# Optimization experiments

Hardware: AMD Instinct MI355X
Metric: run time of the kernel (lower is better)

Reference implementation:

```python
import jax, jax.numpy as jnp
import numpy as np

EMBED = 768
B, S = 8, 2048

def setup_inputs() -> dict:
    key = jax.random.key(0)
    k1, k2, k3, k4 = jax.random.split(key, 4)
    x = jax.random.normal(k1, (B, S, EMBED), dtype=jnp.float32)
    scale = 1.0 / np.sqrt(EMBED)
    Wv = jax.random.normal(k2, (EMBED, EMBED), dtype=jnp.float32) * scale
    Wk = jax.random.normal(k3, (EMBED, EMBED), dtype=jnp.float32) * scale
    Wq = jax.random.normal(k4, (EMBED, EMBED), dtype=jnp.float32) * scale
    mask = jnp.ones((B, S, S), dtype=jnp.int32)
    return {"x": x, "Wv": Wv, "Wk": Wk, "Wq": Wq, "mask": mask}

def reference(x, Wv, Wk, Wq, mask):
    # nn.Linear(E, E, bias=False): y = x @ W.T
    values = jnp.einsum('bse,fe->bsf', x, Wv)
    keys = jnp.einsum('bse,fe->bsf', x, Wk)
    queries = jnp.einsum('bse,fe->bsf', x, Wq)
    energy = jnp.einsum('bqd,bkd->bqk', queries, keys)  # [B,S,S]
    energy = jnp.where(mask == 0, jnp.float32(-1e20), energy)
    attention = jax.nn.softmax(energy / jnp.sqrt(jnp.float32(EMBED)), axis=2)
    out = jnp.einsum('bqk,bkd->bqd', attention, values)
    return out
```

## Files before the change

kernel.cpp:

```cpp
#include <hip/hip_runtime.h>
#include <stdint.h>

#define EMB 768
#define NBATCH 8
#define SEQ 2048
#define M_TOT (NBATCH*SEQ)

using bf16x8 = __attribute__((ext_vector_type(8))) short;
using f32x4  = __attribute__((ext_vector_type(4))) float;

__device__ __forceinline__ short f2bf(float f) {
  __bf16 h = (__bf16)f;
  return __builtin_bit_cast(short, h);
}
__device__ __forceinline__ short f2h(float f) {
  _Float16 h = (_Float16)f;
  return __builtin_bit_cast(short, h);
}
__device__ __forceinline__ float h2f(short s) {
  return (float)__builtin_bit_cast(_Float16, s);
}
__device__ __forceinline__ f32x4 MFMA(bf16x8 a, bf16x8 b, f32x4 c) {
  return __builtin_amdgcn_mfma_f32_16x16x32_bf16(a, b, c, 0, 0, 0);
}
#define GLOAD_LDS16(g, l) __builtin_amdgcn_global_load_lds( \
    (const __attribute__((address_space(1))) unsigned int*)(g), \
    (__attribute__((address_space(3))) unsigned int*)(l), 16, 0, 0)

__global__ __launch_bounds__(256) void cvt_all(
    const float* __restrict__ x, const float* __restrict__ Wq,
    const float* __restrict__ Wk, const float* __restrict__ Wv,
    short* __restrict__ xb, short* __restrict__ Wb)
{
  const size_t NXU = (size_t)M_TOT * EMB / 8;
  const size_t NWU = (size_t)EMB * EMB / 8;
  const size_t total = NXU + 3 * NWU;
  for (size_t u = (size_t)blockIdx.x * 256 + threadIdx.x; u < total;
       u += (size_t)gridDim.x * 256) {
    const float* src; short* dst; size_t off;
    if (u < NXU)            { src = x;  dst = xb;                          off = u; }
    else if (u < NXU+NWU)   { src = Wq; dst = Wb;                          off = u - NXU; }
    else if (u < NXU+2*NWU) { src = Wk; dst = Wb + (size_t)EMB*EMB;        off = u - NXU - NWU; }
    else                    { src = Wv; dst = Wb + (size_t)2*EMB*EMB;      off = u - NXU - 2*NWU; }
    float4 a = reinterpret_cast<const float4*>(src)[off*2];
    float4 c = reinterpret_cast<const float4*>(src)[off*2+1];
    bf16x8 o;
    o[0]=f2bf(a.x); o[1]=f2bf(a.y); o[2]=f2bf(a.z); o[3]=f2bf(a.w);
    o[4]=f2bf(c.x); o[5]=f2bf(c.y); o[6]=f2bf(c.z); o[7]=f2bf(c.w);
    reinterpret_cast<bf16x8*>(dst)[off] = o;
  }
}

#define GEMM_STAGE(As, Bs, asrc, bsrc, lda, ldb)                             \
  {                                                                          \
    _Pragma("unroll")                                                        \
    for (int i = 0; i < 4; ++i) {                                            \
      int slot = i*256 + t;                                                  \
      int row = slot >> 3, g = slot & 7;                                     \
      int gs = (g ^ (row & 7)) << 3;                                         \
      GLOAD_LDS16((asrc) + (size_t)row*(lda) + gs,                           \
                  (char*)&As[0] + (size_t)(i*256 + w*64)*16);                \
      GLOAD_LDS16((bsrc) + (size_t)row*(ldb) + gs,                           \
                  (char*)&Bs[0] + (size_t)(i*256 + w*64)*16);                \
    }                                                                        \
  }

#define GEMM_MFMA(As, Bs)                                                    \
  {                                                                          \
    _Pragma("unroll")                                                        \
    for (int ks = 0; ks < 2; ++ks) {                                         \
      bf16x8 a[4], bb[4];                                                    \
      _Pragma("unroll")                                                      \
      for (int i = 0; i < 4; ++i) {                                          \
        int ra = wm*64 + i*16 + l15;                                         \
        a[i]  = *reinterpret_cast<const bf16x8*>(                            \
                  &As[ra*64 + (((ks*4 + l4) ^ (ra & 7)) << 3)]);             \
        int rb = wn*64 + i*16 + l15;                                         \
        bb[i] = *reinterpret_cast<const bf16x8*>(                            \
                  &Bs[rb*64 + (((ks*4 + l4) ^ (rb & 7)) << 3)]);             \
      }                                                                      \
      _Pragma("unroll")                                                      \
      for (int mi = 0; mi < 4; ++mi)                                         \
        _Pragma("unroll")                                                    \
        for (int ni = 0; ni < 4; ++ni)                                       \
          acc[mi][ni] = MFMA(a[mi], bb[ni], acc[mi][ni]);                    \
    }                                                                        \
  }

__global__ __launch_bounds__(256, 4) void qkv_gemm(
    const short* __restrict__ xb, const short* __restrict__ Wb,
    short* __restrict__ Qb, short* __restrict__ Kb, short* __restrict__ Vt)
{
  __shared__ short As[128*64];
  __shared__ short Bs[128*64];

  const int bid = blockIdx.x;
  const int nb = (bid & 7) * 288 + (bid >> 3);
  const int g = nb / 12, r = nb % 12;
  const int bm = (g / 6) * 4 + r / 3;
  const int bn = (g % 6) * 3 + r % 3;
  const int mbase = bm * 128;

  const short* asrc = xb + (size_t)mbase * EMB;
  const short* bsrc = Wb + (size_t)bn * 128 * EMB;

  const int t = threadIdx.x, lane = t & 63, w = t >> 6;
  const int wm = w >> 1, wn = w & 1, l15 = lane & 15, l4 = lane >> 4;

  f32x4 acc[4][4] = {};

  GEMM_STAGE(As, Bs, asrc, bsrc, EMB, EMB);
  for (int kk = 0; kk < 12; ++kk) {
    asm volatile("s_waitcnt vmcnt(0)" ::: "memory");
    __syncthreads();
    GEMM_MFMA(As, Bs);
    if (kk < 11) {
      __syncthreads();
      GEMM_STAGE(As, Bs, asrc + (kk+1)*64, bsrc + (kk+1)*64, EMB, EMB);
    }
  }

#pragma unroll
  for (int mi = 0; mi < 4; ++mi) {
#pragma unroll
    for (int ni = 0; ni < 4; ++ni) {
      int f = bn * 128 + wn * 64 + ni * 16 + l15;
      int m0 = mbase + wm * 64 + mi * 16 + l4 * 4;
      f32x4 v = acc[mi][ni];
      if (f < 1536) {
        short* dst = (f < 768) ? (Qb + f) : (Kb + (f - 768));
#pragma unroll
        for (int j = 0; j < 4; ++j)
          dst[(size_t)(m0 + j) * EMB] = f2bf(v[j]);
      } else {
        int f2 = f - 1536, bb2 = m0 >> 11, s = m0 & 2047;
        short4 pk = make_short4(f2bf(v[0]), f2bf(v[1]), f2bf(v[2]), f2bf(v[3]));
        *reinterpret_cast<short4*>(&Vt[((size_t)bb2 * EMB + f2) * SEQ + s]) = pk;
      }
    }
  }
}

__global__ __launch_bounds__(256, 4) void energy(
    const short* __restrict__ Qb, const short* __restrict__ Kb,
    short* __restrict__ S)
{
  __shared__ short As[128*64];
  __shared__ short Bs[128*64];

  const int bid = blockIdx.x;
  const int nb = (bid & 7) * 256 + (bid >> 3);
  const int b = nb >> 8;
  const int idx = nb & 255;
  const int sup = idx >> 4, sub = idx & 15;
  const int qt = (sup >> 2) * 4 + (sub >> 2);
  const int kt = (sup & 3) * 4 + (sub & 3);

  const short* asrc = Qb + ((size_t)b*SEQ + qt*128) * EMB;
  const short* bsrc = Kb + ((size_t)b*SEQ + kt*128) * EMB;

  const int t = threadIdx.x, lane = t & 63, w = t >> 6;
  const int wm = w >> 1, wn = w & 1, l15 = lane & 15, l4 = lane >> 4;

  f32x4 acc[4][4] = {};

  GEMM_STAGE(As, Bs, asrc, bsrc, EMB, EMB);
  for (int kk = 0; kk < 12; ++kk) {
    asm volatile("s_waitcnt vmcnt(0)" ::: "memory");
    __syncthreads();
    GEMM_MFMA(As, Bs);
    if (kk < 11) {
      __syncthreads();
      GEMM_STAGE(As, Bs, asrc + (kk+1)*64, bsrc + (kk+1)*64, EMB, EMB);
    }
  }

  const float SCL = 1.4426950408889634f / 27.712812921102035f;
  short* srow = S + (size_t)b * SEQ * SEQ;
#pragma unroll
  for (int mi = 0; mi < 4; ++mi) {
#pragma unroll
    for (int j = 0; j < 4; ++j) {
      int q = qt*128 + wm*64 + mi*16 + l4*4 + j;
#pragma unroll
      for (int ni = 0; ni < 4; ++ni) {
        int k = kt*128 + wn*64 + ni*16 + l15;
        srow[(size_t)q*SEQ + k] = f2h(acc[mi][ni][j] * SCL);
      }
    }
  }
}

__global__ __launch_bounds__(256, 8) void softmax_rows(
    short* __restrict__ S, const int* __restrict__ mask,
    float* __restrict__ invl)
{
  const int w = threadIdx.x >> 6, lane = threadIdx.x & 63;
  const int r = blockIdx.x * 4 + w;
  short* row = S + (size_t)r * SEQ;
  const int4* mrow = reinterpret_cast<const int4*>(mask + (size_t)r * SEQ);

  float f[32];
#pragma unroll
  for (int c = 0; c < 4; ++c) {
    bf16x8 v = *reinterpret_cast<const bf16x8*>(&row[c*512 + lane*8]);
    int4 m0 = mrow[(c*512 + lane*8) >> 2];
    int4 m1 = mrow[((c*512 + lane*8) >> 2) + 1];
    f[c*8+0] = m0.x ? h2f(v[0]) : -30000.0f;
    f[c*8+1] = m0.y ? h2f(v[1]) : -30000.0f;
    f[c*8+2] = m0.z ? h2f(v[2]) : -30000.0f;
    f[c*8+3] = m0.w ? h2f(v[3]) : -30000.0f;
    f[c*8+4] = m1.x ? h2f(v[4]) : -30000.0f;
    f[c*8+5] = m1.y ? h2f(v[5]) : -30000.0f;
    f[c*8+6] = m1.z ? h2f(v[6]) : -30000.0f;
    f[c*8+7] = m1.w ? h2f(v[7]) : -30000.0f;
  }
  float m = -3.0e38f;
#pragma unroll
  for (int i = 0; i < 32; ++i) m = fmaxf(m, f[i]);
#pragma unroll
  for (int off = 32; off >= 1; off >>= 1) m = fmaxf(m, __shfl_xor(m, off));
  float sum = 0.f;
#pragma unroll
  for (int i = 0; i < 32; ++i) {
    f[i] = __builtin_amdgcn_exp2f(f[i] - m);
    sum += f[i];
  }
#pragma unroll
  for (int off = 32; off >= 1; off >>= 1) sum += __shfl_xor(sum, off);

#pragma unroll
  for (int c = 0; c < 4; ++c) {
    bf16x8 o;
#pragma unroll
    for (int j = 0; j < 8; ++j) o[j] = f2bf(f[c*8 + j]);
    *reinterpret_cast<bf16x8*>(&row[c*512 + lane*8]) = o;
  }
  if (lane == 0) invl[r] = 1.0f / sum;
}

__global__ __launch_bounds__(256, 4) void pv(
    const short* __restrict__ P, const short* __restrict__ Vt,
    const float* __restrict__ invl, float* __restrict__ out)
{
  __shared__ short As[128*64];
  __shared__ short Bs[128*64];

  const int bid = blockIdx.x;
  const int nb = (bid & 7) * 96 + (bid >> 3);
  const int b = nb / 96;
  const int idx = nb % 96;
  const int qt = idx / 6, dt = idx % 6;

  const short* asrc = P  + ((size_t)b*SEQ + qt*128) * SEQ;
  const short* bsrc = Vt + ((size_t)b*EMB + dt*128) * SEQ;

  const int t = threadIdx.x, lane = t & 63, w = t >> 6;
  const int wm = w >> 1, wn = w & 1, l15 = lane & 15, l4 = lane >> 4;

  f32x4 acc[4][4] = {};

  GEMM_STAGE(As, Bs, asrc, bsrc, SEQ, SEQ);
  for (int kk = 0; kk < 32; ++kk) {
    asm volatile("s_waitcnt vmcnt(0)" ::: "memory");
    __syncthreads();
    GEMM_MFMA(As, Bs);
    if (kk < 31) {
      __syncthreads();
      GEMM_STAGE(As, Bs, asrc + (kk+1)*64, bsrc + (kk+1)*64, SEQ, SEQ);
    }
  }

#pragma unroll
  for (int mi = 0; mi < 4; ++mi) {
#pragma unroll
    for (int j = 0; j < 4; ++j) {
      int q = qt*128 + wm*64 + mi*16 + l4*4 + j;
      float il = invl[b*SEQ + q];
      float* orow = out + ((size_t)b*SEQ + q) * EMB;
#pragma unroll
      for (int ni = 0; ni < 4; ++ni) {
        int d = dt*128 + wn*64 + ni*16 + l15;
        orow[d] = acc[mi][ni][j] * il;
      }
    }
  }
}

extern "C" void kernel_launch(void* const* d_in, const int* in_sizes, int n_in,
                              void* d_out, int out_size, void* d_ws, size_t ws_size,
                              hipStream_t stream)
{
  (void)in_sizes; (void)n_in; (void)out_size; (void)ws_size;
  const float* x  = (const float*)d_in[0];
  const float* Wv = (const float*)d_in[1];
  const float* Wk = (const float*)d_in[2];
  const float* Wq = (const float*)d_in[3];
  const int* mask = (const int*)d_in[4];
  float* out = (float*)d_out;

  short* Qb = (short*)d_ws;
  short* Kb = Qb + (size_t)M_TOT * EMB;
  short* Vt = Kb + (size_t)M_TOT * EMB;
  short* S  = Vt + (size_t)M_TOT * EMB;
  float* invl = (float*)(S + (size_t)NBATCH * SEQ * SEQ);
  short* xb = S;
  short* Wb = S + (size_t)M_TOT * EMB;

  cvt_all<<<dim3(2048), dim3(256), 0, stream>>>(x, Wq, Wk, Wv, xb, Wb);
  qkv_gemm<<<dim3(2304), dim3(256), 0, stream>>>(xb, Wb, Qb, Kb, Vt);
  energy<<<dim3(2048), dim3(256), 0, stream>>>(Qb, Kb, S);
  softmax_rows<<<dim3(4096), dim3(256), 0, stream>>>(S, mask, invl);
  pv<<<dim3(768), dim3(256), 0, stream>>>(S, Vt, invl, out);
}
```

Before: 245.8 us.

## Use 256x256 double-buffered GEMM tiles with phased loads and MFMA priority

The QKV projection, energy and PV GEMMs now use 512-thread blocks computing 256x256 output tiles, replacing 128x128 tiles. Operands are double-buffered in 128KB of dynamic LDS, and each K step is split into four quarter phases. Each phase issues the next tile's half-loads while MFMAs run, with s_setprio raised around the MFMAs. The aim is more operand reuse per byte loaded and overlap of global-to-LDS traffic with compute. In exchange, only one block fits per CU, grids are much smaller (PV has only 192 blocks), and the kernels depend on a large dynamic LDS launch succeeding.

```diff
diff --git a/kernel.cpp b/kernel.cpp
--- a/kernel.cpp
+++ b/kernel.cpp
@@ -38,10 +38,10 @@
   for (size_t u = (size_t)blockIdx.x * 256 + threadIdx.x; u < total;
        u += (size_t)gridDim.x * 256) {
     const float* src; short* dst; size_t off;
-    if (u < NXU)            { src = x;  dst = xb;                          off = u; }
-    else if (u < NXU+NWU)   { src = Wq; dst = Wb;                          off = u - NXU; }
-    else if (u < NXU+2*NWU) { src = Wk; dst = Wb + (size_t)EMB*EMB;        off = u - NXU - NWU; }
-    else                    { src = Wv; dst = Wb + (size_t)2*EMB*EMB;      off = u - NXU - 2*NWU; }
+    if (u < NXU)            { src = x;  dst = xb;                     off = u; }
+    else if (u < NXU+NWU)   { src = Wq; dst = Wb;                     off = u - NXU; }
+    else if (u < NXU+2*NWU) { src = Wk; dst = Wb + (size_t)EMB*EMB;   off = u - NXU - NWU; }
+    else                    { src = Wv; dst = Wb + (size_t)2*EMB*EMB; off = u - NXU - 2*NWU; }
     float4 a = reinterpret_cast<const float4*>(src)[off*2];
     float4 c = reinterpret_cast<const float4*>(src)[off*2+1];
     bf16x8 o;
@@ -51,143 +51,152 @@
   }
 }
 
-#define GEMM_STAGE(As, Bs, asrc, bsrc, lda, ldb)                             \
-  {                                                                          \
-    _Pragma("unroll")                                                        \
-    for (int i = 0; i < 4; ++i) {                                            \
-      int slot = i*256 + t;                                                  \
-      int row = slot >> 3, g = slot & 7;                                     \
-      int gs = (g ^ (row & 7)) << 3;                                         \
-      GLOAD_LDS16((asrc) + (size_t)row*(lda) + gs,                           \
-                  (char*)&As[0] + (size_t)(i*256 + w*64)*16);                \
-      GLOAD_LDS16((bsrc) + (size_t)row*(ldb) + gs,                           \
-                  (char*)&Bs[0] + (size_t)(i*256 + w*64)*16);                \
-    }                                                                        \
-  }
-
-#define GEMM_MFMA(As, Bs)                                                    \
-  {                                                                          \
-    _Pragma("unroll")                                                        \
-    for (int ks = 0; ks < 2; ++ks) {                                         \
-      bf16x8 a[4], bb[4];                                                    \
-      _Pragma("unroll")                                                      \
-      for (int i = 0; i < 4; ++i) {                                          \
-        int ra = wm*64 + i*16 + l15;                                         \
-        a[i]  = *reinterpret_cast<const bf16x8*>(                            \
-                  &As[ra*64 + (((ks*4 + l4) ^ (ra & 7)) << 3)]);             \
-        int rb = wn*64 + i*16 + l15;                                         \
-        bb[i] = *reinterpret_cast<const bf16x8*>(                            \
-                  &Bs[rb*64 + (((ks*4 + l4) ^ (rb & 7)) << 3)]);             \
-      }                                                                      \
-      _Pragma("unroll")                                                      \
-      for (int mi = 0; mi < 4; ++mi)                                         \
-        _Pragma("unroll")                                                    \
-        for (int ni = 0; ni < 4; ++ni)                                       \
-          acc[mi][ni] = MFMA(a[mi], bb[ni], acc[mi][ni]);                    \
-    }                                                                        \
-  }
-
-__global__ __launch_bounds__(256, 4) void qkv_gemm(
+#define STAGE_HALF(ldsb, src, ld, k0, h)                                      \
+  { _Pragma("unroll") for (int i_ = 0; i_ < 2; ++i_) {                        \
+      int slot_ = i_*512 + t;                                                 \
+      int row_ = (h)*128 + (slot_ >> 3), g_ = slot_ & 7;                      \
+      GLOAD_LDS16((src) + (size_t)row_*(ld) + (k0) + ((g_ ^ (row_ & 7)) << 3),\
+                  (ldsb) + (h)*16384 + (size_t)(i_*512 + w*64)*16); } }
+
+#define PHASE(mh, nh, W, ...)                                                 \
+  {                                                                           \
+    bf16x8 af_[2][4], bfr_[2][2];                                             \
+    _Pragma("unroll") for (int ks_ = 0; ks_ < 2; ++ks_) {                     \
+      _Pragma("unroll") for (int mi_ = 0; mi_ < 4; ++mi_) {                   \
+        int r_ = (mh)*128 + wm*64 + mi_*16 + l15;                             \
+        af_[ks_][mi_] = *reinterpret_cast<const bf16x8*>(                     \
+            Ar + r_*64 + (((ks_*4 + l4) ^ (r_ & 7)) << 3));                   \
+      }                                                                       \
+      _Pragma("unroll") for (int ni_ = 0; ni_ < 2; ++ni_) {                   \
+        int r_ = (nh)*128 + wn*32 + ni_*16 + l15;                             \
+        bfr_[ks_][ni_] = *reinterpret_cast<const bf16x8*>(                    \
+            Br + r_*64 + (((ks_*4 + l4) ^ (r_ & 7)) << 3));                   \
+      }                                                                       \
+    }                                                                         \
+    __VA_ARGS__                                                               \
+    asm volatile("s_waitcnt vmcnt(" #W ")" ::: "memory");                     \
+    asm volatile("s_barrier" ::: "memory");                                   \
+    __builtin_amdgcn_s_setprio(1);                                            \
+    _Pragma("unroll") for (int ks_ = 0; ks_ < 2; ++ks_)                       \
+      _Pragma("unroll") for (int mi_ = 0; mi_ < 4; ++mi_)                     \
+        _Pragma("unroll") for (int ni_ = 0; ni_ < 2; ++ni_)                   \
+          acc[mh][nh][mi_][ni_] =                                             \
+              MFMA(af_[ks_][mi_], bfr_[ks_][ni_], acc[mh][nh][mi_][ni_]);     \
+    __builtin_amdgcn_s_setprio(0);                                            \
+    asm volatile("s_barrier" ::: "memory");                                   \
+  }
+
+#define GEMM_PRO_BODY(asrc, bsrc, lda, ldb, NT)                               \
+  short* const A0p = (short*)smem;                                            \
+  short* const B0p = (short*)(smem + 32768);                                  \
+  short* const A1p = (short*)(smem + 65536);                                  \
+  short* const B1p = (short*)(smem + 98304);                                  \
+  f32x4 acc[2][2][4][2] = {};                                                 \
+  STAGE_HALF((char*)A0p, asrc, lda, 0, 0);                                    \
+  STAGE_HALF((char*)B0p, bsrc, ldb, 0, 0);                                    \
+  STAGE_HALF((char*)B0p, bsrc, ldb, 0, 1);                                    \
+  STAGE_HALF((char*)A0p, asrc, lda, 0, 1);                                    \
+  asm volatile("s_waitcnt vmcnt(4)" ::: "memory");                            \
+  asm volatile("s_barrier" ::: "memory");                                     \
+  for (int T = 0; T < (NT) - 1; ++T) {                                        \
+    short* Ar = (T & 1) ? A1p : A0p;                                          \
+    short* Br = (T & 1) ? B1p : B0p;                                          \
+    char* Aw = (char*)((T & 1) ? A0p : A1p);                                  \
+    char* Bw = (char*)((T & 1) ? B0p : B1p);                                  \
+    const int nk = (T + 1) * 64;                                              \
+    PHASE(0,0, 4, STAGE_HALF(Aw, asrc, lda, nk, 0))                           \
+    PHASE(0,1, 4, STAGE_HALF(Bw, bsrc, ldb, nk, 0))                           \
+    PHASE(1,0, 4, STAGE_HALF(Bw, bsrc, ldb, nk, 1))                           \
+    PHASE(1,1, 4, STAGE_HALF(Aw, asrc, lda, nk, 1))                           \
+  }                                                                           \
+  {                                                                           \
+    short* Ar = (((NT)-1) & 1) ? A1p : A0p;                                   \
+    short* Br = (((NT)-1) & 1) ? B1p : B0p;                                   \
+    asm volatile("s_waitcnt vmcnt(0)" ::: "memory");     \
+    asm volatile("s_barrier" ::: "memory");                                   \
+    PHASE(0,0, 0)                                                             \
+    PHASE(0,1, 0)                                                             \
+    PHASE(1,0, 0)                                                             \
+    PHASE(1,1, 0)                                                             \
+  }
+
+__global__ __launch_bounds__(512, 2) void qkv_gemm(
     const short* __restrict__ xb, const short* __restrict__ Wb,
     short* __restrict__ Qb, short* __restrict__ Kb, short* __restrict__ Vt)
 {
-  __shared__ short As[128*64];
-  __shared__ short Bs[128*64];
+  extern __shared__ char smem[];
+  const int t = threadIdx.x, lane = t & 63, w = t >> 6;
+  const int wm = w >> 2, wn = w & 3, l15 = lane & 15, l4 = lane >> 4;
 
   const int bid = blockIdx.x;
-  const int nb = (bid & 7) * 288 + (bid >> 3);
-  const int g = nb / 12, r = nb % 12;
-  const int bm = (g / 6) * 4 + r / 3;
-  const int bn = (g % 6) * 3 + r % 3;
-  const int mbase = bm * 128;
-
-  const short* asrc = xb + (size_t)mbase * EMB;
-  const short* bsrc = Wb + (size_t)bn * 128 * EMB;
-
-  const int t = threadIdx.x, lane = t & 63, w = t >> 6;
-  const int wm = w >> 1, wn = w & 1, l15 = lane & 15, l4 = lane >> 4;
-
-  f32x4 acc[4][4] = {};
-
-  GEMM_STAGE(As, Bs, asrc, bsrc, EMB, EMB);
-  for (int kk = 0; kk < 12; ++kk) {
-    asm volatile("s_waitcnt vmcnt(0)" ::: "memory");
-    __syncthreads();
-    GEMM_MFMA(As, Bs);
-    if (kk < 11) {
-      __syncthreads();
-      GEMM_STAGE(As, Bs, asrc + (kk+1)*64, bsrc + (kk+1)*64, EMB, EMB);
+  const int nb = (bid & 7) * 72 + (bid >> 3);
+  const int bm = nb / 9, bn = nb % 9;
+
+  const short* asrc = xb + (size_t)bm * 256 * EMB;
+  const short* bsrc = Wb + (size_t)bn * 256 * EMB;
+
+  GEMM_PRO_BODY(asrc, bsrc, EMB, EMB, 12)
+
+#pragma unroll
+  for (int mh = 0; mh < 2; ++mh)
+#pragma unroll
+  for (int nh = 0; nh < 2; ++nh)
+#pragma unroll
+  for (int mi = 0; mi < 4; ++mi)
+#pragma unroll
+  for (int ni = 0; ni < 2; ++ni) {
+    int f  = bn*256 + nh*128 + wn*32 + ni*16 + l15;
+    int m0 = bm*256 + mh*128 + wm*64 + mi*16 + l4*4;
+    f32x4 v = acc[mh][nh][mi][ni];
+    if (f < 1536) {
+      short* dst = (f < 768) ? (Qb + f) : (Kb + (f - 768));
+#pragma unroll
+      for (int j = 0; j < 4; ++j)
+        dst[(size_t)(m0 + j) * EMB] = f2bf(v[j]);
+    } else {
+      int f2 = f - 1536, bb2 = m0 >> 11, s = m0 & 2047;
+      short4 pk = make_short4(f2bf(v[0]), f2bf(v[1]), f2bf(v[2]), f2bf(v[3]));
+      *reinterpret_cast<short4*>(&Vt[((size_t)bb2 * EMB + f2) * SEQ + s]) = pk;
     }
   }
-
-#pragma unroll
-  for (int mi = 0; mi < 4; ++mi) {
-#pragma unroll
-    for (int ni = 0; ni < 4; ++ni) {
-      int f = bn * 128 + wn * 64 + ni * 16 + l15;
-      int m0 = mbase + wm * 64 + mi * 16 + l4 * 4;
-      f32x4 v = acc[mi][ni];
-      if (f < 1536) {
-        short* dst = (f < 768) ? (Qb + f) : (Kb + (f - 768));
-#pragma unroll
-        for (int j = 0; j < 4; ++j)
-          dst[(size_t)(m0 + j) * EMB] = f2bf(v[j]);
-      } else {
-        int f2 = f - 1536, bb2 = m0 >> 11, s = m0 & 2047;
-        short4 pk = make_short4(f2bf(v[0]), f2bf(v[1]), f2bf(v[2]), f2bf(v[3]));
-        *reinterpret_cast<short4*>(&Vt[((size_t)bb2 * EMB + f2) * SEQ + s]) = pk;
-      }
-    }
-  }
-}
-
-__global__ __launch_bounds__(256, 4) void energy(
+}
+
+__global__ __launch_bounds__(512, 2) void energy(
     const short* __restrict__ Qb, const short* __restrict__ Kb,
     short* __restrict__ S)
 {
-  __shared__ short As[128*64];
-  __shared__ short Bs[128*64];
+  extern __shared__ char smem[];
+  const int t = threadIdx.x, lane = t & 63, w = t >> 6;
+  const int wm = w >> 2, wn = w & 3, l15 = lane & 15, l4 = lane >> 4;
 
   const int bid = blockIdx.x;
-  const int nb = (bid & 7) * 256 + (bid >> 3);
-  const int b = nb >> 8;
-  const int idx = nb & 255;
-  const int sup = idx >> 4, sub = idx & 15;
-  const int qt = (sup >> 2) * 4 + (sub >> 2);
-  const int kt = (sup & 3) * 4 + (sub & 3);
-
-  const short* asrc = Qb + ((size_t)b*SEQ + qt*128) * EMB;
-  const short* bsrc = Kb + ((size_t)b*SEQ + kt*128) * EMB;
-
-  const int t = threadIdx.x, lane = t & 63, w = t >> 6;
-  const int wm = w >> 1, wn = w & 1, l15 = lane & 15, l4 = lane >> 4;
-
-  f32x4 acc[4][4] = {};
-
-  GEMM_STAGE(As, Bs, asrc, bsrc, EMB, EMB);
-  for (int kk = 0; kk < 12; ++kk) {
-    asm volatile("s_waitcnt vmcnt(0)" ::: "memory");
-    __syncthreads();
-    GEMM_MFMA(As, Bs);
-    if (kk < 11) {
-      __syncthreads();
-      GEMM_STAGE(As, Bs, asrc + (kk+1)*64, bsrc + (kk+1)*64, EMB, EMB);
-    }
-  }
+  const int nb = (bid & 7) * 64 + (bid >> 3);
+  const int b = nb >> 6;
+  const int idx = nb & 63;
+  const int sup = idx >> 2, sub = idx & 3;
+  const int qt = (sup >> 2) * 2 + (sub >> 1);
+  const int kt = (sup & 3) * 2 + (sub & 1);
+
+  const short* asrc = Qb + ((size_t)b*SEQ + qt*256) * EMB;
+  const short* bsrc = Kb + ((size_t)b*SEQ + kt*256) * EMB;
+
+  GEMM_PRO_BODY(asrc, bsrc, EMB, EMB, 12)
 
   const float SCL = 1.4426950408889634f / 27.712812921102035f;
   short* srow = S + (size_t)b * SEQ * SEQ;
 #pragma unroll
-  for (int mi = 0; mi < 4; ++mi) {
-#pragma unroll
-    for (int j = 0; j < 4; ++j) {
-      int q = qt*128 + wm*64 + mi*16 + l4*4 + j;
-#pragma unroll
-      for (int ni = 0; ni < 4; ++ni) {
-        int k = kt*128 + wn*64 + ni*16 + l15;
-        srow[(size_t)q*SEQ + k] = f2h(acc[mi][ni][j] * SCL);
-      }
-    }
+  for (int mh = 0; mh < 2; ++mh)
+#pragma unroll
+  for (int nh = 0; nh < 2; ++nh)
+#pragma unroll
+  for (int mi = 0; mi < 4; ++mi)
+#pragma unroll
+  for (int ni = 0; ni < 2; ++ni)
+#pragma unroll
+  for (int j = 0; j < 4; ++j) {
+    int q = qt*256 + mh*128 + wm*64 + mi*16 + l4*4 + j;
+    int k = kt*256 + nh*128 + wn*32 + ni*16 + l15;
+    srow[(size_t)q*SEQ + k] = f2h(acc[mh][nh][mi][ni][j] * SCL);
   }
 }
 
@@ -239,50 +248,40 @@
   if (lane == 0) invl[r] = 1.0f / sum;
 }
 
-__global__ __launch_bounds__(256, 4) void pv(
+__global__ __launch_bounds__(512, 2) void pv(
     const short* __restrict__ P, const short* __restrict__ Vt,
     const float* __restrict__ invl, float* __restrict__ out)
 {
-  __shared__ short As[128*64];
-  __shared__ short Bs[128*64];
+  extern __shared__ char smem[];
+  const int t = threadIdx.x, lane = t & 63, w = t >> 6;
+  const int wm = w >> 2, wn = w & 3, l15 = lane & 15, l4 = lane >> 4;
 
   const int bid = blockIdx.x;
-  const int nb = (bid & 7) * 96 + (bid >> 3);
-  const int b = nb / 96;
-  const int idx = nb % 96;
-  const int qt = idx / 6, dt = idx % 6;
-
-  const short* asrc = P  + ((size_t)b*SEQ + qt*128) * SEQ;
-  const short* bsrc = Vt + ((size_t)b*EMB + dt*128) * SEQ;
-
-  const int t = threadIdx.x, lane = t & 63, w = t >> 6;
-  const int wm = w >> 1, wn = w & 1, l15 = lane & 15, l4 = lane >> 4;
-
-  f32x4 acc[4][4] = {};
-
-  GEMM_STAGE(As, Bs, asrc, bsrc, SEQ, SEQ);
-  for (int kk = 0; kk < 32; ++kk) {
-    asm volatile("s_waitcnt vmcnt(0)" ::: "memory");
-    __syncthreads();
-    GEMM_MFMA(As, Bs);
-    if (kk < 31) {
-      __syncthreads();
-      GEMM_STAGE(As, Bs, asrc + (kk+1)*64, bsrc + (kk+1)*64, SEQ, SEQ);
-    }
-  }
-
-#pragma unroll
-  for (int mi = 0; mi < 4; ++mi) {
-#pragma unroll
-    for (int j = 0; j < 4; ++j) {
-      int q = qt*128 + wm*64 + mi*16 + l4*4 + j;
-      float il = invl[b*SEQ + q];
-      float* orow = out + ((size_t)b*SEQ + q) * EMB;
-#pragma unroll
-      for (int ni = 0; ni < 4; ++ni) {
-        int d = dt*128 + wn*64 + ni*16 + l15;
-        orow[d] = acc[mi][ni][j] * il;
-      }
+  const int nb = (bid & 7) * 24 + (bid >> 3);
+  const int b = nb / 24;
+  const int idx = nb % 24;
+  const int qt = idx / 3, dt = idx % 3;
+
+  const short* asrc = P  + ((size_t)b*SEQ + qt*256) * SEQ;
+  const short* bsrc = Vt + ((size_t)b*EMB + dt*256) * SEQ;
+
+  GEMM_PRO_BODY(asrc, bsrc, SEQ, SEQ, 32)
+
+#pragma unroll
+  for (int mh = 0; mh < 2; ++mh)
+#pragma unroll
+  for (int nh = 0; nh < 2; ++nh)
+#pragma unroll
+  for (int mi = 0; mi < 4; ++mi)
+#pragma unroll
+  for (int j = 0; j < 4; ++j) {
+    int q = qt*256 + mh*128 + wm*64 + mi*16 + l4*4 + j;
+    float il = invl[b*SEQ + q];
+    float* orow = out + ((size_t)b*SEQ + q) * EMB;
+#pragma unroll
+    for (int ni = 0; ni < 2; ++ni) {
+      int d = dt*256 + nh*128 + wn*32 + ni*16 + l15;
+      orow[d] = acc[mh][nh][mi][ni][j] * il;
     }
   }
 }
@@ -308,8 +307,8 @@
   short* Wb = S + (size_t)M_TOT * EMB;
 
   cvt_all<<<dim3(2048), dim3(256), 0, stream>>>(x, Wq, Wk, Wv, xb, Wb);
-  qkv_gemm<<<dim3(2304), dim3(256), 0, stream>>>(xb, Wb, Qb, Kb, Vt);
-  energy<<<dim3(2048), dim3(256), 0, stream>>>(Qb, Kb, S);
+  qkv_gemm<<<dim3(576), dim3(512), 131072, stream>>>(xb, Wb, Qb, Kb, Vt);
+  energy<<<dim3(512), dim3(512), 131072, stream>>>(Qb, Kb, S);
   softmax_rows<<<dim3(4096), dim3(256), 0, stream>>>(S, mask, invl);
-  pv<<<dim3(768), dim3(256), 0, stream>>>(S, Vt, invl, out);
-}
+  pv<<<dim3(192), dim3(512), 131072, stream>>>(S, Vt, invl, out);
+}
```

New measurement: 272.1 us. 1.11x slower.
